# Performance work log

Hardware: AMD Instinct MI355X
Metric: run time of the kernel (lower is better)

Reference implementation:

```python
import jax, jax.numpy as jnp
import numpy as np

B, T, F, L, E, H, A, V = 64, 32, 512, 196, 512, 512, 512, 10000


def setup_inputs() -> dict:
    key = jax.random.key(0)
    ks = jax.random.split(key, 24)
    s = 0.02
    features = jax.random.normal(ks[0], (B, F, L), dtype=jnp.float32)
    captions = jax.random.randint(ks[1], (B, T), 0, V)
    lengths = jnp.sort(jax.random.randint(ks[2], (B,), 2, T + 1))[::-1]
    lengths = lengths.at[0].set(T)  # ensure max(decode_lengths) == T-1 (static)
    return {
        "features": features,
        "captions": captions,
        "lengths": lengths,
        "W_emb": jax.random.normal(ks[3], (V, E)) * s,
        "W_enc": jax.random.normal(ks[4], (A, F)) * s,
        "b_enc": jnp.zeros((A,)),
        "W_dec": jax.random.normal(ks[5], (A, H)) * s,
        "b_dec": jnp.zeros((A,)),
        "W_full": jax.random.normal(ks[6], (1, A)) * s,
        "b_full": jnp.zeros((1,)),
        "W_fbeta": jax.random.normal(ks[7], (F, H)) * s,
        "b_fbeta": jnp.zeros((F,)),
        "W_ih": jax.random.normal(ks[8], (4 * H, E + F)) * s,
        "W_hh": jax.random.normal(ks[9], (4 * H, H)) * s,
        "b_ih": jnp.zeros((4 * H,)),
        "b_hh": jnp.zeros((4 * H,)),
        "W_out": jax.random.normal(ks[10], (V, H)) * s,
        "b_out": jnp.zeros((V,)),
        "W_init_h": jax.random.normal(ks[11], (H, F)) * s,
        "b_init_h": jnp.zeros((H,)),
        "W_init_c": jax.random.normal(ks[12], (H, F)) * s,
        "b_init_c": jnp.zeros((H,)),
    }


def reference(features, captions, lengths, W_emb, W_enc, b_enc, W_dec, b_dec,
              W_full, b_full, W_fbeta, b_fbeta, W_ih, W_hh, b_ih, b_hh,
              W_out, b_out, W_init_h, b_init_h, W_init_c, b_init_c):
    Bv, Fv, Lv = features.shape
    Tmax = captions.shape[1] - 1  # max(decode_lengths), static (lengths[0]==T)
    feat_r = features.reshape(Bv, -1, Fv)          # [B, L, F] (torch .view semantics)
    en_att = feat_r @ W_enc.T + b_enc              # [B, L, A], step-invariant
    mean_f = features.mean(axis=2)                 # [B, F]
    h0 = mean_f @ W_init_h.T + b_init_h            # [B, H]
    c0 = mean_f @ W_init_c.T + b_init_c
    emb = W_emb[captions]                          # [B, T, E]
    dec_len = lengths - 1                          # [B]

    def step(carry, xs):
        h, c = carry
        emb_t, i = xs
        de = h @ W_dec.T + b_dec                                   # [B, A]
        full = (jnp.tanh(en_att + de[:, None, :]) @ W_full.T)[..., 0] + b_full[0]  # [B, L]
        alpha = jax.nn.softmax(full, axis=1)                       # [B, L]
        z = jnp.einsum('blf,bl->bf', feat_r, alpha)                # [B, F]
        z = z * jax.nn.sigmoid(h @ W_fbeta.T + b_fbeta)
        x = jnp.concatenate([emb_t, z], axis=1)                    # [B, E+F]
        gates = x @ W_ih.T + b_ih + h @ W_hh.T + b_hh              # [B, 4H]
        ig, fg, gg, og = jnp.split(gates, 4, axis=1)
        c_new = jax.nn.sigmoid(fg) * c + jax.nn.sigmoid(ig) * jnp.tanh(gg)
        h_new = jax.nn.sigmoid(og) * jnp.tanh(c_new)
        out = h_new @ W_out.T + b_out                              # [B, V] (dropout: eval)
        active = (dec_len > i)[:, None]                            # ragged mask
        h = jnp.where(active, h_new, h)
        c = jnp.where(active, c_new, c)
        pred = jnp.where(active, out, 0.0)
        alpha_m = jnp.where(active, alpha, 0.0)
        return (h, c), (pred, alpha_m)

    emb_steps = jnp.swapaxes(emb[:, :Tmax, :], 0, 1)               # [Tmax, B, E]
    (_, _), (preds, alphas) = jax.lax.scan(step, (h0, c0), (emb_steps, jnp.arange(Tmax)))
    predictions = jnp.swapaxes(preds, 0, 1)                        # [B, Tmax, V]
    alphas = jnp.swapaxes(alphas, 0, 1)                            # [B, Tmax, L]
    return predictions, alphas
```

## Files before the change

### kernel.cpp

```cpp
#include <hip/hip_runtime.h>


typedef unsigned short ushort_t;
typedef __attribute__((ext_vector_type(8))) short short8;
typedef __attribute__((ext_vector_type(4))) float f32x4;

__device__ __forceinline__ float bf2f(ushort_t u) {
    unsigned x = ((unsigned)u) << 16;
    float f;
    __builtin_memcpy(&f, &x, 4);
    return f;
}
__device__ __forceinline__ ushort_t f2bf(float f) {
    unsigned x;
    __builtin_memcpy(&x, &f, 4);
    unsigned r = (x + 0x7fffu + ((x >> 16) & 1u)) >> 16;
    return (ushort_t)r;
}
__device__ __forceinline__ float sigmoidf_(float x) { return 1.f / (1.f + __expf(-x)); }
__device__ __forceinline__ float tanh_fast(float x) {
    float e = __expf(2.f * x);
    return 1.f - 2.f / (e + 1.f);
}
__device__ __forceinline__ float wred_sum(float v) {
    #pragma unroll
    for (int m = 32; m; m >>= 1) v += __shfl_xor(v, m, 64);
    return v;
}
__device__ __forceinline__ float wred_max(float v) {
    #pragma unroll
    for (int m = 32; m; m >>= 1) v = fmaxf(v, __shfl_xor(v, m, 64));
    return v;
}

__device__ __forceinline__ float aload_f(const float* p) {
    return __hip_atomic_load((float*)p, __ATOMIC_RELAXED, __HIP_MEMORY_SCOPE_AGENT);
}
__device__ __forceinline__ void astore_f(float* p, float v) {
    __hip_atomic_store(p, v, __ATOMIC_RELAXED, __HIP_MEMORY_SCOPE_AGENT);
}
__device__ __forceinline__ unsigned aload_u(const unsigned* p) {
    return __hip_atomic_load((unsigned*)p, __ATOMIC_RELAXED, __HIP_MEMORY_SCOPE_AGENT);
}
__device__ __forceinline__ void astore_u(unsigned* p, unsigned v) {
    __hip_atomic_store(p, v, __ATOMIC_RELAXED, __HIP_MEMORY_SCOPE_AGENT);
}
__device__ __forceinline__ int aload_i(const int* p) {
    return __hip_atomic_load((int*)p, __ATOMIC_RELAXED, __HIP_MEMORY_SCOPE_AGENT);
}

#define KEXP2 2.8853901817779268f

__global__ void detect_kernel(const unsigned* __restrict__ feat_raw, int* __restrict__ flag,
                              int* __restrict__ slots) {
    int lane = threadIdx.x;
    #pragma unroll
    for (int i = 0; i < 8; ++i) slots[lane + i * 64] = 0;
    unsigned u = feat_raw[lane];
    unsigned e = (u >> 7) & 0xffu;
    bool bf_like = (e >= 105 && e <= 133);
    unsigned long long m = __ballot(bf_like);
    if (lane == 0) *flag = (__popcll(m) >= 40) ? 0 : 1;
}

#define NCVT 19
struct CvtArgs {
    const void* src[NCVT];
    void* dst[NCVT];
    int n[NCVT];
};

__global__ __launch_bounds__(256) void convert_kernel(CvtArgs a, const int* __restrict__ flag) {
    const int ai = blockIdx.y;
    const int n = a.n[ai];
    const int base = (blockIdx.x * 256 + threadIdx.x) * 8;
    if (base >= n) return;
    ushort_t* dst = (ushort_t*)a.dst[ai];
    if (*flag) {
        const float* s = (const float*)a.src[ai];
        #pragma unroll
        for (int i = 0; i < 8; ++i) {
            int idx = base + i;
            if (idx < n) dst[idx] = f2bf(s[idx]);
        }
    } else {
        const ushort_t* s = (const ushort_t*)a.src[ai];
        #pragma unroll
        for (int i = 0; i < 8; ++i) {
            int idx = base + i;
            if (idx < n) dst[idx] = s[idx];
        }
    }
}

__global__ __launch_bounds__(256) void embrows_kernel(const void* __restrict__ Wemb,
                                                      const int* __restrict__ captions,
                                                      const int* __restrict__ flag,
                                                      ushort_t* __restrict__ emb_c) {
    const int tb = blockIdx.x;
    const int t = tb >> 6, b = tb & 63;
    const int cap = captions[b * 32 + t];
    const int e0 = threadIdx.x;
    if (*flag) {
        const float* s = (const float*)Wemb + cap * 512;
        emb_c[tb * 512 + e0] = f2bf(s[e0]);
        emb_c[tb * 512 + e0 + 256] = f2bf(s[e0 + 256]);
    } else {
        const ushort_t* s = (const ushort_t*)Wemb + cap * 512;
        emb_c[tb * 512 + e0] = s[e0];
        emb_c[tb * 512 + e0 + 256] = s[e0 + 256];
    }
}

__global__ void prepw2_kernel(const ushort_t* __restrict__ wf, const ushort_t* __restrict__ bfc,
                              float* __restrict__ w2) {
    int tid = threadIdx.x;
    float w = bf2f(wf[tid]);
    w2[tid] = -2.f * w;
    float s = wred_sum(w);
    __shared__ float r8[8];
    if ((tid & 63) == 0) r8[tid >> 6] = s;
    __syncthreads();
    if (tid == 0) {
        float tot = r8[0] + r8[1] + r8[2] + r8[3] + r8[4] + r8[5] + r8[6] + r8[7];
        w2[512] = tot + bf2f(bfc[0]);
    }
}

template <class AROW, class BROW, class EPI>
__device__ __forceinline__ void gemm_tile(AROW arow, BROW brow, EPI epi) {
    __shared__ __align__(16) ushort_t As[64][40];
    __shared__ __align__(16) ushort_t Bs[64][40];
    const int tid = threadIdx.x;
    const int row = tid >> 2, ks = (tid & 3) << 3;
    const int wave = tid >> 6, lane = tid & 63;
    const int quad = lane >> 4, l15 = lane & 15;
    f32x4 acc[4];
    #pragma unroll
    for (int s = 0; s < 4; ++s) acc[s] = (f32x4){0.f, 0.f, 0.f, 0.f};
    const ushort_t* ap = arow(row);
    const ushort_t* bp = brow(row);
    for (int k0 = 0; k0 < 512; k0 += 32) {
        short8 av = {0, 0, 0, 0, 0, 0, 0, 0};
        short8 bv = {0, 0, 0, 0, 0, 0, 0, 0};
        if (ap) av = *(const short8*)(ap + k0 + ks);
        if (bp) bv = *(const short8*)(bp + k0 + ks);
        __syncthreads();
        *(short8*)&As[row][ks] = av;
        *(short8*)&Bs[row][ks] = bv;
        __syncthreads();
        short8 af = *(const short8*)&As[(wave << 4) + l15][quad << 3];
        #pragma unroll
        for (int s = 0; s < 4; ++s) {
            short8 bfr = *(const short8*)&Bs[(s << 4) + l15][quad << 3];
            acc[s] = __builtin_amdgcn_mfma_f32_16x16x32_bf16(af, bfr, acc[s], 0, 0, 0);
        }
    }
    epi((wave << 4) + (quad << 2), l15, acc);
}

__global__ __launch_bounds__(256) void mean_kernel(const ushort_t* __restrict__ features,
                                                   ushort_t* __restrict__ mean_bf) {
    const int b = blockIdx.x;
    const int wave = threadIdx.x >> 6, lane = threadIdx.x & 63;
    const ushort_t* fb = features + b * 512 * 196;
    for (int f = wave; f < 512; f += 4) {
        const ushort_t* r = fb + f * 196;
        float s = bf2f(r[lane]) + bf2f(r[lane + 64]) + bf2f(r[lane + 128]);
        if (lane < 4) s += bf2f(r[lane + 192]);
        s = wred_sum(s);
        if (lane == 0) mean_bf[b * 512 + f] = f2bf(s * (1.f / 196.f));
    }
}

__global__ __launch_bounds__(256) void init_kernel(
    const ushort_t* __restrict__ mean_bf, const ushort_t* __restrict__ Winh,
    const ushort_t* __restrict__ binh, const ushort_t* __restrict__ Winc,
    const ushort_t* __restrict__ binc, ushort_t* __restrict__ h_bf,
    float* __restrict__ cbuf) {
    const int n0 = blockIdx.x << 6;
    gemm_tile(
        [&](int r) { return mean_bf + r * 512; },
        [&](int r) {
            int n = n0 + r;
            return (n < 512) ? (Winh + n * 512) : (Winc + (n - 512) * 512);
        },
        [&](int mb, int l15, const f32x4* acc) {
            #pragma unroll
            for (int s = 0; s < 4; ++s) {
                int n = n0 + (s << 4) + l15;
                #pragma unroll
                for (int r = 0; r < 4; ++r) {
                    int b = mb + r;
                    if (n < 512)
                        h_bf[b * 512 + n] = f2bf(acc[s][r] + bf2f(binh[n]));
                    else
                        cbuf[b * 512 + (n - 512)] = acc[s][r] + bf2f(binc[n - 512]);
                }
            }
        });
}

__global__ __launch_bounds__(256) void enatt_kernel(const ushort_t* __restrict__ feat,
                                                    const ushort_t* __restrict__ Wenc,
                                                    const ushort_t* __restrict__ benc,
                                                    ushort_t* __restrict__ en_att) {
    const int m0 = blockIdx.y << 6, n0 = blockIdx.x << 6;
    gemm_tile(
        [&](int r) { return feat + (m0 + r) * 512; },
        [&](int r) { return Wenc + (n0 + r) * 512; },
        [&](int mb, int l15, const f32x4* acc) {
            #pragma unroll
            for (int s = 0; s < 4; ++s) {
                int n = n0 + (s << 4) + l15;
                float bias = bf2f(benc[n]);
                #pragma unroll
                for (int r = 0; r < 4; ++r) {
                    int m = m0 + mb + r;
                    en_att[m * 512 + n] = f2bf(acc[s][r] + bias);
                }
            }
        });
}

__global__ __launch_bounds__(256) void ec_kernel(const ushort_t* __restrict__ emb_c,
                                                 const ushort_t* __restrict__ Wih,
                                                 const ushort_t* __restrict__ bih,
                                                 const ushort_t* __restrict__ bhh,
                                                 float* __restrict__ ec) {
    const int t = blockIdx.y, n0 = blockIdx.x << 6;
    gemm_tile(
        [&](int r) { return emb_c + (t * 64 + r) * 512; },
        [&](int r) { return Wih + (n0 + r) * 1024; },
        [&](int mb, int l15, const f32x4* acc) {
            #pragma unroll
            for (int s = 0; s < 4; ++s) {
                int j = n0 + (s << 4) + l15;
                float bias = bf2f(bih[j]) + bf2f(bhh[j]);
                #pragma unroll
                for (int r = 0; r < 4; ++r) {
                    int b = mb + r;
                    ec[(t * 64 + b) * 2048 + j] = acc[s][r] + bias;
                }
            }
        });
}

__device__ __forceinline__ void gbar(int* slots, int e) {
    asm volatile("s_waitcnt vmcnt(0)" ::: "memory");
    __syncthreads();
    const int tid = threadIdx.x;
    if (tid == 0)
        __hip_atomic_store(slots + blockIdx.x, e, __ATOMIC_RELAXED,
                           __HIP_MEMORY_SCOPE_AGENT);
    if (blockIdx.x == 0) {
        if (tid < 64) {
            for (;;) {
                int a = aload_i(slots + tid);
                int b = aload_i(slots + tid + 64);
                int c = aload_i(slots + tid + 128);
                int d = aload_i(slots + tid + 192);
                if (__all(min(min(a, b), min(c, d)) >= e)) break;
                __builtin_amdgcn_s_sleep(1);
            }
            asm volatile("" ::: "memory");
            if (tid == 0)
                __hip_atomic_store(slots + 320, e, __ATOMIC_RELAXED,
                                   __HIP_MEMORY_SCOPE_AGENT);
        }
    } else if (tid == 0) {
        while (aload_i(slots + 320) < e) __builtin_amdgcn_s_sleep(1);
    }
    __syncthreads();
}

struct LoopArgs {
    const ushort_t* W3c;
    const ushort_t* bdec;
    const ushort_t* bfb;
    const ushort_t* en_att;
    const ushort_t* feat;
    const ushort_t* Wih;
    const float* w2;
    const float* ec;
    const int* lengths;
    const int* flag;
    ushort_t* h_bf;
    ushort_t* z_bf;
    ushort_t* H_all;
    float* cbuf;
    float* deK;
    float* fgate;
    float* hh;
    float* fullv;
    void* out_base;
    int* bar;
};

__global__ __launch_bounds__(512, 2) void loop_kernel(LoopArgs A) {
    const int blk = blockIdx.x, tid = threadIdx.x;
    const int wave = tid >> 6, lane = tid & 63;
    const int quad = lane >> 4, l15 = lane & 15;

    __shared__ __align__(16) ushort_t enS[49 * 512];
    __shared__ __align__(16) ushort_t ftS[196 * 128];
    __shared__ __align__(16) ushort_t AsL[16][520];
    __shared__ float smem[2048];
    __shared__ float red8[16];

    const int f32o = *A.flag;
    const int bB = blk >> 2;
    const int qB = blk & 3;
    const int lenB = A.lengths[bB];

    const int mtA = blk & 3;
    const int ntbA = (blk >> 2) << 3;
    const int b0A = mtA << 4;
    const int lenA = A.lengths[b0A + l15];

    const int dtC = blk >> 2;
    const int b0C = (blk & 3) << 4;
    const int lenC = A.lengths[b0C + l15];

    unsigned* h_u32 = (unsigned*)A.h_bf;
    unsigned* z_u32 = (unsigned*)A.z_bf;

    float w2r[8];
    {
        f32x4 w0 = *(const f32x4*)(A.w2 + lane * 8);
        f32x4 w1 = *(const f32x4*)(A.w2 + lane * 8 + 4);
        w2r[0] = w0[0]; w2r[1] = w0[1]; w2r[2] = w0[2]; w2r[3] = w0[3];
        w2r[4] = w1[0]; w2r[5] = w1[1]; w2r[6] = w1[2]; w2r[7] = w1[3];
    }
    const float fullc = A.w2[512];

    {
        const short8* src = (const short8*)(A.en_att + ((size_t)bB * 196 + qB * 49) * 512);
        short8* dst = (short8*)enS;
        for (int i = tid; i < 49 * 64; i += 512) dst[i] = src[i];
        const ushort_t* fsrc = A.feat + (size_t)bB * 100352 + qB * 128;
        short8* fdst = (short8*)ftS;
        for (int i = tid; i < 196 * 16; i += 512) {
            int l = i >> 4, c = i & 15;
            fdst[i] = *(const short8*)(fsrc + l * 512 + c * 8);
        }
    }

    int bt = 0;
    for (int t = 0; t < 31; ++t) {
        if (blk < 96) {
            bool anyact = __any(lenA - 1 > t);
            if (anyact) {
                for (int i = tid; i < 4096; i += 512) {
                    int r = i >> 8, c = i & 255;
                    unsigned v = aload_u(h_u32 + (b0A + r) * 256 + c);
                    *(unsigned*)&AsL[r][c << 1] = v;
                }
                __syncthreads();
                const int nt = ntbA + wave;
                const ushort_t* br = A.W3c + ((nt << 4) + l15) * 512 + (quad << 3);
                const ushort_t* arl = &AsL[l15][quad << 3];
                f32x4 acc = {0.f, 0.f, 0.f, 0.f};
                #pragma unroll
                for (int k0 = 0; k0 < 512; k0 += 32)
                    acc = __builtin_amdgcn_mfma_f32_16x16x32_bf16(
                        *(const short8*)(arl + k0), *(const short8*)(br + k0), acc, 0, 0, 0);
                const int n = (nt << 4) + l15;
                #pragma unroll
                for (int r = 0; r < 4; ++r) {
                    const int b = b0A + (quad << 2) + r;
                    float v = acc[r];
                    if (n < 512)
                        astore_f(A.deK + b * 512 + n, (v + bf2f(A.bdec[n])) * KEXP2);
                    else if (n < 1024)
                        astore_f(A.fgate + b * 512 + (n - 512),
                                 sigmoidf_(v + bf2f(A.bfb[n - 512])));
                    else
                        astore_f(A.hh + b * 2048 + (n - 1024), v);
                }
            }
        }
        ++bt; gbar(A.bar, bt);

        if ((lenB - 1) > t) {
            float dkr[8];
            const float* dk = A.deK + bB * 512 + lane * 8;
            #pragma unroll
            for (int j = 0; j < 8; ++j) dkr[j] = aload_f(dk + j);
            for (int i = wave; i < 49; i += 8) {
                short8 ev = *(const short8*)(enS + i * 512 + lane * 8);
                float acc = 0.f;
                #pragma unroll
                for (int j = 0; j < 8; ++j) {
                    float e2 = __builtin_amdgcn_exp2f(
                        fmaf(bf2f((ushort_t)ev[j]), KEXP2, dkr[j]));
                    acc = fmaf(w2r[j], __builtin_amdgcn_rcpf(e2 + 1.f), acc);
                }
                acc = wred_sum(acc);
                if (lane == 0) astore_f(A.fullv + bB * 196 + qB * 49 + i, acc + fullc);
            }
        }
        ++bt; gbar(A.bar, bt);

        {
            const bool act = (lenB - 1) > t;
            const size_t aoff = 19840000ull + ((size_t)bB * 31 + t) * 196;
            if (!act) {
                if (qB == 0 && tid < 196) {
                    if (f32o) ((float*)A.out_base)[aoff + tid] = 0.f;
                    else ((ushort_t*)A.out_base)[aoff + tid] = 0;
                }
            } else {
                float v = (tid < 196) ? aload_f(A.fullv + bB * 196 + tid) : -1e30f;
                float wm = wred_max(v);
                if (lane == 0) red8[wave] = wm;
                __syncthreads();
                float mx = fmaxf(fmaxf(fmaxf(red8[0], red8[1]), fmaxf(red8[2], red8[3])),
                                 fmaxf(fmaxf(red8[4], red8[5]), fmaxf(red8[6], red8[7])));
                float e = (tid < 196) ? __expf(v - mx) : 0.f;
                float sw = wred_sum(e);
                if (lane == 0) red8[8 + wave] = sw;
                __syncthreads();
                float tot = red8[8] + red8[9] + red8[10] + red8[11] +
                            red8[12] + red8[13] + red8[14] + red8[15];
                float inv = 1.f / tot;
                float a = e * inv;
                if (tid < 196) {
                    smem[tid] = a;
                    if (qB == 0) {
                        if (f32o) ((float*)A.out_base)[aoff + tid] = a;
                        else ((ushort_t*)A.out_base)[aoff + tid] = f2bf(a);
                    }
                }
                __syncthreads();
                const int fl = tid & 127, g = tid >> 7;
                float zacc = 0.f;
                #pragma unroll 4
                for (int l = g; l < 196; l += 4)
                    zacc = fmaf(smem[l], bf2f(ftS[l * 128 + fl]), zacc);
                smem[256 + (g << 7) + fl] = zacc;
                __syncthreads();
                if (tid < 64) {
                    const int f0l = tid << 1;
                    float z0 = smem[256 + f0l] + smem[384 + f0l] +
                               smem[512 + f0l] + smem[640 + f0l];
                    float z1 = smem[257 + f0l] + smem[385 + f0l] +
                               smem[513 + f0l] + smem[641 + f0l];
                    const int f0 = (qB << 7) + f0l;
                    z0 *= aload_f(A.fgate + bB * 512 + f0);
                    z1 *= aload_f(A.fgate + bB * 512 + f0 + 1);
                    unsigned zp = (unsigned)f2bf(z0) | ((unsigned)f2bf(z1) << 16);
                    astore_u(z_u32 + bB * 256 + (f0 >> 1), zp);
                }
            }
        }
        ++bt; gbar(A.bar, bt);

        if (blk < 128) {
            bool anyact = __any(lenC - 1 > t);
            if (anyact) {
                float pe[8], ph[8];
                #pragma unroll
                for (int k = 0; k < 8; ++k) { pe[k] = 0.f; ph[k] = 0.f; }
                if (tid < 128) {
                    const int bl = tid >> 3, p = tid & 7;
                    const int bE = b0C + bl;
                    const int dimE = (dtC << 4) + (p << 1);
                    const int eb = (t * 64 + bE) * 2048, hb = bE * 2048;
                    pe[0] = A.ec[eb + dimE];         pe[1] = A.ec[eb + dimE + 1];
                    pe[2] = A.ec[eb + 512 + dimE];   pe[3] = A.ec[eb + 512 + dimE + 1];
                    pe[4] = A.ec[eb + 1024 + dimE];  pe[5] = A.ec[eb + 1024 + dimE + 1];
                    pe[6] = A.ec[eb + 1536 + dimE];  pe[7] = A.ec[eb + 1536 + dimE + 1];
                    ph[0] = aload_f(A.hh + hb + dimE);
                    ph[1] = aload_f(A.hh + hb + dimE + 1);
                    ph[2] = aload_f(A.hh + hb + 512 + dimE);
                    ph[3] = aload_f(A.hh + hb + 512 + dimE + 1);
                    ph[4] = aload_f(A.hh + hb + 1024 + dimE);
                    ph[5] = aload_f(A.hh + hb + 1024 + dimE + 1);
                    ph[6] = aload_f(A.hh + hb + 1536 + dimE);
                    ph[7] = aload_f(A.hh + hb + 1536 + dimE + 1);
                }
                for (int i = tid; i < 4096; i += 512) {
                    int r = i >> 8, c = i & 255;
                    unsigned v = aload_u(z_u32 + (b0C + r) * 256 + c);
                    *(unsigned*)&AsL[r][c << 1] = v;
                }
                __syncthreads();
                const int g = wave & 3, kh = wave >> 2;
                const int j = (g << 9) + (dtC << 4) + l15;
                const ushort_t* br = A.Wih + j * 1024 + 512 + (kh << 8) + (quad << 3);
                const ushort_t* arl = &AsL[l15][(kh << 8) + (quad << 3)];
                f32x4 acc = {0.f, 0.f, 0.f, 0.f};
                #pragma unroll
                for (int k0 = 0; k0 < 256; k0 += 32)
                    acc = __builtin_amdgcn_mfma_f32_16x16x32_bf16(
                        *(const short8*)(arl + k0), *(const short8*)(br + k0), acc, 0, 0, 0);
                #pragma unroll
                for (int r = 0; r < 4; ++r)
                    smem[(wave << 8) + (((quad << 2) + r) << 4) + l15] = acc[r];
                __syncthreads();
                if (tid < 128) {
                    const int bl = tid >> 3, p = tid & 7;
                    const int b = b0C + bl;
                    const int i0 = (bl << 4) + (p << 1);
                    const int dim = (dtC << 4) + (p << 1);
                    float ig0 = smem[i0] + smem[1024 + i0] + pe[0] + ph[0];
                    float ig1 = smem[i0 + 1] + smem[1025 + i0] + pe[1] + ph[1];
                    float fg0 = smem[256 + i0] + smem[1280 + i0] + pe[2] + ph[2];
                    float fg1 = smem[257 + i0] + smem[1281 + i0] + pe[3] + ph[3];
                    float gg0 = smem[512 + i0] + smem[1536 + i0] + pe[4] + ph[4];
                    float gg1 = smem[513 + i0] + smem[1537 + i0] + pe[5] + ph[5];
                    float og0 = smem[768 + i0] + smem[1792 + i0] + pe[6] + ph[6];
                    float og1 = smem[769 + i0] + smem[1793 + i0] + pe[7] + ph[7];
                    float co0 = A.cbuf[b * 512 + dim];
                    float co1 = A.cbuf[b * 512 + dim + 1];
                    float cn0 = sigmoidf_(fg0) * co0 + sigmoidf_(ig0) * tanh_fast(gg0);
                    float hn0 = sigmoidf_(og0) * tanh_fast(cn0);
                    float cn1 = sigmoidf_(fg1) * co1 + sigmoidf_(ig1) * tanh_fast(gg1);
                    float hn1 = sigmoidf_(og1) * tanh_fast(cn1);
                    unsigned hp = (unsigned)f2bf(hn0) | ((unsigned)f2bf(hn1) << 16);
                    *(unsigned*)&A.H_all[(t * 64 + b) * 512 + dim] = hp;
                    if (A.lengths[b] - 1 > t) {
                        A.cbuf[b * 512 + dim] = cn0;
                        A.cbuf[b * 512 + dim + 1] = cn1;
                        astore_u(h_u32 + b * 256 + (dim >> 1), hp);
                    }
                }
            }
        }
        ++bt; gbar(A.bar, bt);
    }
}

__global__ __launch_bounds__(256) void preds_kernel(
    const ushort_t* __restrict__ H_all, const ushort_t* __restrict__ Wout,
    const ushort_t* __restrict__ bout, const int* __restrict__ lengths,
    const int* __restrict__ flag, void* __restrict__ out_base) {
    const int t = blockIdx.x, n0 = blockIdx.y << 6;
    const int f32o = *flag;
    gemm_tile(
        [&](int r) { return H_all + (t * 64 + r) * 512; },
        [&](int r) -> const ushort_t* {
            int n = n0 + r;
            return (n < 10000) ? (Wout + n * 512) : (const ushort_t*)nullptr;
        },
        [&](int mb, int l15, const f32x4* acc) {
            #pragma unroll
            for (int s = 0; s < 4; ++s) {
                int n = n0 + (s << 4) + l15;
                if (n >= 10000) continue;
                float bias = bf2f(bout[n]);
                #pragma unroll
                for (int r = 0; r < 4; ++r) {
                    int b = mb + r;
                    bool act = lengths[b] > t + 1;
                    float val = act ? (acc[s][r] + bias) : 0.f;
                    size_t off = (size_t)b * 310000 + t * 10000 + n;
                    if (f32o) ((float*)out_base)[off] = val;
                    else ((ushort_t*)out_base)[off] = act ? f2bf(val) : (ushort_t)0;
                }
            }
        });
}

extern "C" void kernel_launch(void* const* d_in, const int* in_sizes, int n_in,
                              void* d_out, int out_size, void* d_ws, size_t ws_size,
                              hipStream_t stream) {
    const void* features = d_in[0];
    const int* captions = (const int*)d_in[1];
    const int* lengths = (const int*)d_in[2];
    const void* W_emb = d_in[3];

    char* ws = (char*)d_ws;
    size_t o = 0;
    auto alloc = [&](size_t bytes) {
        size_t r = o;
        o += (bytes + 255) & ~(size_t)255;
        return r;
    };
    ushort_t* feat_c  = (ushort_t*)(ws + alloc(6422528ull * 2));
    ushort_t* Wenc_c  = (ushort_t*)(ws + alloc(262144ull * 2));
    ushort_t* benc_c  = (ushort_t*)(ws + alloc(512 * 2));
    ushort_t* W3c     = (ushort_t*)(ws + alloc(3072ull * 512 * 2));
    ushort_t* bdec_c  = (ushort_t*)(ws + alloc(512 * 2));
    ushort_t* wfull_c = (ushort_t*)(ws + alloc(512 * 2));
    ushort_t* bfull_c = (ushort_t*)(ws + alloc(2));
    ushort_t* bfb_c   = (ushort_t*)(ws + alloc(512 * 2));
    ushort_t* Wih_c   = (ushort_t*)(ws + alloc(2097152ull * 2));
    ushort_t* bih_c   = (ushort_t*)(ws + alloc(2048 * 2));
    ushort_t* bhh_c   = (ushort_t*)(ws + alloc(2048 * 2));
    ushort_t* Wout_c  = (ushort_t*)(ws + alloc(5120000ull * 2));
    ushort_t* bout_c  = (ushort_t*)(ws + alloc(10000 * 2));
    ushort_t* Winh_c  = (ushort_t*)(ws + alloc(262144ull * 2));
    ushort_t* binh_c  = (ushort_t*)(ws + alloc(512 * 2));
    ushort_t* Winc_c  = (ushort_t*)(ws + alloc(262144ull * 2));
    ushort_t* binc_c  = (ushort_t*)(ws + alloc(512 * 2));
    ushort_t* emb_c   = (ushort_t*)(ws + alloc(1984ull * 512 * 2));
    ushort_t* en_att  = (ushort_t*)(ws + alloc(12544ull * 512 * 2));
    float*    ec      = (float*)(ws + alloc(1984ull * 2048 * 4));
    ushort_t* H_all   = (ushort_t*)(ws + alloc(1984ull * 512 * 2));
    ushort_t* h_bf    = (ushort_t*)(ws + alloc(64 * 512 * 2));
    float*    cbuf    = (float*)(ws + alloc(64 * 512 * 4));
    float*    deK     = (float*)(ws + alloc(64 * 512 * 4));
    float*    fgate   = (float*)(ws + alloc(64 * 512 * 4));
    float*    hh      = (float*)(ws + alloc(64ull * 2048 * 4));
    ushort_t* z_bf    = (ushort_t*)(ws + alloc(64 * 512 * 2));
    ushort_t* mean_bf = (ushort_t*)(ws + alloc(64 * 512 * 2));
    float*    fullv   = (float*)(ws + alloc(64 * 196 * 4));
    float*    w2buf   = (float*)(ws + alloc(513 * 4));
    int*      flag    = (int*)(ws + alloc(256));
    int*      bar     = (int*)(ws + alloc(512 * 4));

    detect_kernel<<<1, 64, 0, stream>>>((const unsigned*)features, flag, bar);

    CvtArgs ca;
    const void* srcs[NCVT] = {features, d_in[4], d_in[5], d_in[6], d_in[7], d_in[8],
                              d_in[9], d_in[10], d_in[11], d_in[12], d_in[13], d_in[14],
                              d_in[15], d_in[16], d_in[17], d_in[18], d_in[19], d_in[20],
                              d_in[21]};
    void* dsts[NCVT] = {feat_c, Wenc_c, benc_c, W3c , bdec_c, wfull_c, bfull_c,
                        W3c + 262144 , bfb_c, Wih_c, W3c + 524288 ,
                        bih_c, bhh_c, Wout_c, bout_c, Winh_c, binh_c, Winc_c, binc_c};
    int ns[NCVT] = {6422528, 262144, 512, 262144, 512, 512, 1, 262144, 512,
                    2097152, 1048576, 2048, 2048, 5120000, 10000, 262144, 512,
                    262144, 512};
    for (int i = 0; i < NCVT; ++i) {
        ca.src[i] = srcs[i];
        ca.dst[i] = dsts[i];
        ca.n[i] = ns[i];
    }
    convert_kernel<<<dim3(3136, NCVT), 256, 0, stream>>>(ca, flag);
    embrows_kernel<<<1984, 256, 0, stream>>>(W_emb, captions, flag, emb_c);
    prepw2_kernel<<<1, 512, 0, stream>>>(wfull_c, bfull_c, w2buf);

    mean_kernel<<<64, 256, 0, stream>>>(feat_c, mean_bf);
    init_kernel<<<16, 256, 0, stream>>>(mean_bf, Winh_c, binh_c, Winc_c, binc_c,
                                        h_bf, cbuf);
    enatt_kernel<<<dim3(8, 196), 256, 0, stream>>>(feat_c, Wenc_c, benc_c, en_att);
    ec_kernel<<<dim3(32, 31), 256, 0, stream>>>(emb_c, Wih_c, bih_c, bhh_c, ec);

    LoopArgs la;
    la.W3c = W3c; la.bdec = bdec_c; la.bfb = bfb_c;
    la.en_att = en_att; la.feat = feat_c; la.Wih = Wih_c;
    la.w2 = w2buf; la.ec = ec; la.lengths = lengths; la.flag = flag;
    la.h_bf = h_bf; la.z_bf = z_bf; la.H_all = H_all;
    la.cbuf = cbuf; la.deK = deK; la.fgate = fgate; la.hh = hh;
    la.fullv = fullv; la.out_base = d_out; la.bar = bar;
    loop_kernel<<<256, 512, 0, stream>>>(la);

    preds_kernel<<<dim3(31, 157), 256, 0, stream>>>(H_all, Wout_c, bout_c, lengths,
                                                    flag, d_out);
}
```

Baseline: 1.189 ms.

## Replace grid-wide barriers with per-batch-group flag synchronization in recurrent loop

The persistent loop kernel stops using four grid-wide barriers per timestep. Its 256 blocks are split into 4 independent groups of 64, each owning 16 batch rows, and the groups coordinate through producer/consumer flag counters. Each group runs only to its own maximum decode length, and the attention logits are computed whole in each block instead of exchanged through global memory. This removes the global barrier latency and skips steps for shorter groups, at the cost of redundantly recomputing attention scores over all 196 locations per block, three quarters of them read from global memory.

```diff
diff --git a/kernel.cpp b/kernel.cpp
--- a/kernel.cpp
+++ b/kernel.cpp
@@ -48,14 +48,17 @@
 __device__ __forceinline__ int aload_i(const int* p) {
     return __hip_atomic_load((int*)p, __ATOMIC_RELAXED, __HIP_MEMORY_SCOPE_AGENT);
 }
+__device__ __forceinline__ void astore_i(int* p, int v) {
+    __hip_atomic_store(p, v, __ATOMIC_RELAXED, __HIP_MEMORY_SCOPE_AGENT);
+}
 
 #define KEXP2 2.8853901817779268f
 
 __global__ void detect_kernel(const unsigned* __restrict__ feat_raw, int* __restrict__ flag,
-                              int* __restrict__ slots) {
+                              int* __restrict__ flags) {
     int lane = threadIdx.x;
     #pragma unroll
-    for (int i = 0; i < 8; ++i) slots[lane + i * 64] = 0;
+    for (int i = 0; i < 8; ++i) flags[lane + i * 64] = 0;
     unsigned u = feat_raw[lane];
     unsigned e = (u >> 7) & 0xffu;
     bool bf_like = (e >= 105 && e <= 133);
@@ -246,34 +249,6 @@
         });
 }
 
-__device__ __forceinline__ void gbar(int* slots, int e) {
-    asm volatile("s_waitcnt vmcnt(0)" ::: "memory");
-    __syncthreads();
-    const int tid = threadIdx.x;
-    if (tid == 0)
-        __hip_atomic_store(slots + blockIdx.x, e, __ATOMIC_RELAXED,
-                           __HIP_MEMORY_SCOPE_AGENT);
-    if (blockIdx.x == 0) {
-        if (tid < 64) {
-            for (;;) {
-                int a = aload_i(slots + tid);
-                int b = aload_i(slots + tid + 64);
-                int c = aload_i(slots + tid + 128);
-                int d = aload_i(slots + tid + 192);
-                if (__all(min(min(a, b), min(c, d)) >= e)) break;
-                __builtin_amdgcn_s_sleep(1);
-            }
-            asm volatile("" ::: "memory");
-            if (tid == 0)
-                __hip_atomic_store(slots + 320, e, __ATOMIC_RELAXED,
-                                   __HIP_MEMORY_SCOPE_AGENT);
-        }
-    } else if (tid == 0) {
-        while (aload_i(slots + 320) < e) __builtin_amdgcn_s_sleep(1);
-    }
-    __syncthreads();
-}
-
 struct LoopArgs {
     const ushort_t* W3c;
     const ushort_t* bdec;
@@ -292,35 +267,34 @@
     float* deK;
     float* fgate;
     float* hh;
-    float* fullv;
     void* out_base;
-    int* bar;
+    int* flags;
 };
 
 __global__ __launch_bounds__(512, 2) void loop_kernel(LoopArgs A) {
     const int blk = blockIdx.x, tid = threadIdx.x;
     const int wave = tid >> 6, lane = tid & 63;
     const int quad = lane >> 4, l15 = lane & 15;
+    const int g = blk >> 6, local = blk & 63;
+    int* fbase = A.flags + g * 128;
 
     __shared__ __align__(16) ushort_t enS[49 * 512];
     __shared__ __align__(16) ushort_t ftS[196 * 128];
     __shared__ __align__(16) ushort_t AsL[16][520];
     __shared__ float smem[2048];
+    __shared__ float fullS[200];
     __shared__ float red8[16];
 
     const int f32o = *A.flag;
-    const int bB = blk >> 2;
-    const int qB = blk & 3;
+    const int b0 = g << 4;
+    const int Tg = A.lengths[b0] - 1;
+
+    const bool roleA = local < 24;
+    const int bB = b0 + (local >> 2);
+    const int qB = local & 3;
     const int lenB = A.lengths[bB];
-
-    const int mtA = blk & 3;
-    const int ntbA = (blk >> 2) << 3;
-    const int b0A = mtA << 4;
-    const int lenA = A.lengths[b0A + l15];
-
-    const int dtC = blk >> 2;
-    const int b0C = (blk & 3) << 4;
-    const int lenC = A.lengths[b0C + l15];
+    const bool roleC = local < 32;
+    const int dtC = local;
 
     unsigned* h_u32 = (unsigned*)A.h_bf;
     unsigned* z_u32 = (unsigned*)A.z_bf;
@@ -346,72 +320,84 @@
         }
     }
 
-    int bt = 0;
-    for (int t = 0; t < 31; ++t) {
-        if (blk < 96) {
-            bool anyact = __any(lenA - 1 > t);
-            if (anyact) {
-                for (int i = tid; i < 4096; i += 512) {
-                    int r = i >> 8, c = i & 255;
-                    unsigned v = aload_u(h_u32 + (b0A + r) * 256 + c);
-                    *(unsigned*)&AsL[r][c << 1] = v;
-                }
-                __syncthreads();
-                const int nt = ntbA + wave;
-                const ushort_t* br = A.W3c + ((nt << 4) + l15) * 512 + (quad << 3);
-                const ushort_t* arl = &AsL[l15][quad << 3];
-                f32x4 acc = {0.f, 0.f, 0.f, 0.f};
-                #pragma unroll
-                for (int k0 = 0; k0 < 512; k0 += 32)
-                    acc = __builtin_amdgcn_mfma_f32_16x16x32_bf16(
-                        *(const short8*)(arl + k0), *(const short8*)(br + k0), acc, 0, 0, 0);
-                const int n = (nt << 4) + l15;
-                #pragma unroll
-                for (int r = 0; r < 4; ++r) {
-                    const int b = b0A + (quad << 2) + r;
-                    float v = acc[r];
-                    if (n < 512)
-                        astore_f(A.deK + b * 512 + n, (v + bf2f(A.bdec[n])) * KEXP2);
-                    else if (n < 1024)
-                        astore_f(A.fgate + b * 512 + (n - 512),
-                                 sigmoidf_(v + bf2f(A.bfb[n - 512])));
-                    else
-                        astore_f(A.hh + b * 2048 + (n - 1024), v);
-                }
-            }
-        }
-        ++bt; gbar(A.bar, bt);
-
-        if ((lenB - 1) > t) {
-            float dkr[8];
-            const float* dk = A.deK + bB * 512 + lane * 8;
-            #pragma unroll
-            for (int j = 0; j < 8; ++j) dkr[j] = aload_f(dk + j);
-            for (int i = wave; i < 49; i += 8) {
-                short8 ev = *(const short8*)(enS + i * 512 + lane * 8);
-                float acc = 0.f;
-                #pragma unroll
-                for (int j = 0; j < 8; ++j) {
-                    float e2 = __builtin_amdgcn_exp2f(
-                        fmaf(bf2f((ushort_t)ev[j]), KEXP2, dkr[j]));
-                    acc = fmaf(w2r[j], __builtin_amdgcn_rcpf(e2 + 1.f), acc);
-                }
-                acc = wred_sum(acc);
-                if (lane == 0) astore_f(A.fullv + bB * 196 + qB * 49 + i, acc + fullc);
-            }
-        }
-        ++bt; gbar(A.bar, bt);
+    for (int t = 0; t < Tg; ++t) {
+        if (roleA) {
+            if (wave == 0 && t > 0) {
+                const int* fp = fbase + (lane & 31);
+                for (;;) {
+                    if (__all(aload_i(fp) >= t)) break;
+                    __builtin_amdgcn_s_sleep(1);
+                }
+                asm volatile("" ::: "memory");
+            }
+            __syncthreads();
+            for (int i = tid; i < 4096; i += 512) {
+                int r = i >> 8, c = i & 255;
+                *(unsigned*)&AsL[r][c << 1] = aload_u(h_u32 + ((b0 + r) << 8) + c);
+            }
+            __syncthreads();
+            const int nt = local * 8 + wave;
+            const ushort_t* br = A.W3c + ((nt << 4) + l15) * 512 + (quad << 3);
+            const ushort_t* arl = &AsL[l15][quad << 3];
+            f32x4 acc = {0.f, 0.f, 0.f, 0.f};
+            #pragma unroll
+            for (int k0 = 0; k0 < 512; k0 += 32)
+                acc = __builtin_amdgcn_mfma_f32_16x16x32_bf16(
+                    *(const short8*)(arl + k0), *(const short8*)(br + k0), acc, 0, 0, 0);
+            const int n = (nt << 4) + l15;
+            #pragma unroll
+            for (int r = 0; r < 4; ++r) {
+                const int b = b0 + (quad << 2) + r;
+                float v = acc[r];
+                if (n < 512)
+                    astore_f(A.deK + b * 512 + n, (v + bf2f(A.bdec[n])) * KEXP2);
+                else if (n < 1024)
+                    astore_f(A.fgate + b * 512 + (n - 512),
+                             sigmoidf_(v + bf2f(A.bfb[n - 512])));
+                else
+                    astore_f(A.hh + b * 2048 + (n - 1024), v);
+            }
+            asm volatile("s_waitcnt vmcnt(0)" ::: "memory");
+            __syncthreads();
+            if (tid == 0) astore_i(fbase + 32 + local, t + 1);
+        }
 
         {
+            if (wave == 0) {
+                const int* fp = fbase + 32 + (lane & 7);
+                for (;;) {
+                    if (__all(aload_i(fp) >= t + 1)) break;
+                    __builtin_amdgcn_s_sleep(1);
+                }
+                asm volatile("" ::: "memory");
+            }
+            __syncthreads();
             const bool act = (lenB - 1) > t;
             const size_t aoff = 19840000ull + ((size_t)bB * 31 + t) * 196;
-            if (!act) {
-                if (qB == 0 && tid < 196) {
-                    if (f32o) ((float*)A.out_base)[aoff + tid] = 0.f;
-                    else ((ushort_t*)A.out_base)[aoff + tid] = 0;
-                }
-            } else {
-                float v = (tid < 196) ? aload_f(A.fullv + bB * 196 + tid) : -1e30f;
+            if (act) {
+                float dkr[8];
+                const float* dk = A.deK + bB * 512 + lane * 8;
+                #pragma unroll
+                for (int j = 0; j < 8; ++j) dkr[j] = aload_f(dk + j);
+                const ushort_t* enb = A.en_att + (size_t)bB * 100352;
+                const int lp0 = qB * 49;
+                for (int l = wave; l < 196; l += 8) {
+                    const ushort_t* er = (l >= lp0 && l < lp0 + 49)
+                                             ? (enS + (l - lp0) * 512)
+                                             : (enb + l * 512);
+                    short8 ev = *(const short8*)(er + lane * 8);
+                    float acc = 0.f;
+                    #pragma unroll
+                    for (int j = 0; j < 8; ++j) {
+                        float e2 = __builtin_amdgcn_exp2f(
+                            fmaf(bf2f((ushort_t)ev[j]), KEXP2, dkr[j]));
+                        acc = fmaf(w2r[j], __builtin_amdgcn_rcpf(e2 + 1.f), acc);
+                    }
+                    acc = wred_sum(acc);
+                    if (lane == 0) fullS[l] = acc + fullc;
+                }
+                __syncthreads();
+                float v = (tid < 196) ? fullS[tid] : -1e30f;
                 float wm = wred_max(v);
                 if (lane == 0) red8[wave] = wm;
                 __syncthreads();
@@ -426,19 +412,19 @@
                 float inv = 1.f / tot;
                 float a = e * inv;
                 if (tid < 196) {
-                    smem[tid] = a;
+                    fullS[tid] = a;
                     if (qB == 0) {
                         if (f32o) ((float*)A.out_base)[aoff + tid] = a;
                         else ((ushort_t*)A.out_base)[aoff + tid] = f2bf(a);
                     }
                 }
                 __syncthreads();
-                const int fl = tid & 127, g = tid >> 7;
+                const int fl = tid & 127, gq = tid >> 7;
                 float zacc = 0.f;
                 #pragma unroll 4
-                for (int l = g; l < 196; l += 4)
-                    zacc = fmaf(smem[l], bf2f(ftS[l * 128 + fl]), zacc);
-                smem[256 + (g << 7) + fl] = zacc;
+                for (int l = gq; l < 196; l += 4)
+                    zacc = fmaf(fullS[l], bf2f(ftS[l * 128 + fl]), zacc);
+                smem[256 + (gq << 7) + fl] = zacc;
                 __syncthreads();
                 if (tid < 64) {
                     const int f0l = tid << 1;
@@ -452,83 +438,111 @@
                     unsigned zp = (unsigned)f2bf(z0) | ((unsigned)f2bf(z1) << 16);
                     astore_u(z_u32 + bB * 256 + (f0 >> 1), zp);
                 }
-            }
-        }
-        ++bt; gbar(A.bar, bt);
-
-        if (blk < 128) {
-            bool anyact = __any(lenC - 1 > t);
-            if (anyact) {
-                float pe[8], ph[8];
-                #pragma unroll
-                for (int k = 0; k < 8; ++k) { pe[k] = 0.f; ph[k] = 0.f; }
-                if (tid < 128) {
-                    const int bl = tid >> 3, p = tid & 7;
-                    const int bE = b0C + bl;
-                    const int dimE = (dtC << 4) + (p << 1);
-                    const int eb = (t * 64 + bE) * 2048, hb = bE * 2048;
-                    pe[0] = A.ec[eb + dimE];         pe[1] = A.ec[eb + dimE + 1];
-                    pe[2] = A.ec[eb + 512 + dimE];   pe[3] = A.ec[eb + 512 + dimE + 1];
-                    pe[4] = A.ec[eb + 1024 + dimE];  pe[5] = A.ec[eb + 1024 + dimE + 1];
-                    pe[6] = A.ec[eb + 1536 + dimE];  pe[7] = A.ec[eb + 1536 + dimE + 1];
-                    ph[0] = aload_f(A.hh + hb + dimE);
-                    ph[1] = aload_f(A.hh + hb + dimE + 1);
-                    ph[2] = aload_f(A.hh + hb + 512 + dimE);
-                    ph[3] = aload_f(A.hh + hb + 512 + dimE + 1);
-                    ph[4] = aload_f(A.hh + hb + 1024 + dimE);
-                    ph[5] = aload_f(A.hh + hb + 1024 + dimE + 1);
-                    ph[6] = aload_f(A.hh + hb + 1536 + dimE);
-                    ph[7] = aload_f(A.hh + hb + 1536 + dimE + 1);
-                }
-                for (int i = tid; i < 4096; i += 512) {
-                    int r = i >> 8, c = i & 255;
-                    unsigned v = aload_u(z_u32 + (b0C + r) * 256 + c);
-                    *(unsigned*)&AsL[r][c << 1] = v;
-                }
-                __syncthreads();
-                const int g = wave & 3, kh = wave >> 2;
-                const int j = (g << 9) + (dtC << 4) + l15;
-                const ushort_t* br = A.Wih + j * 1024 + 512 + (kh << 8) + (quad << 3);
-                const ushort_t* arl = &AsL[l15][(kh << 8) + (quad << 3)];
-                f32x4 acc = {0.f, 0.f, 0.f, 0.f};
-                #pragma unroll
-                for (int k0 = 0; k0 < 256; k0 += 32)
-                    acc = __builtin_amdgcn_mfma_f32_16x16x32_bf16(
-                        *(const short8*)(arl + k0), *(const short8*)(br + k0), acc, 0, 0, 0);
-                #pragma unroll
-                for (int r = 0; r < 4; ++r)
-                    smem[(wave << 8) + (((quad << 2) + r) << 4) + l15] = acc[r];
-                __syncthreads();
-                if (tid < 128) {
-                    const int bl = tid >> 3, p = tid & 7;
-                    const int b = b0C + bl;
-                    const int i0 = (bl << 4) + (p << 1);
-                    const int dim = (dtC << 4) + (p << 1);
-                    float ig0 = smem[i0] + smem[1024 + i0] + pe[0] + ph[0];
-                    float ig1 = smem[i0 + 1] + smem[1025 + i0] + pe[1] + ph[1];
-                    float fg0 = smem[256 + i0] + smem[1280 + i0] + pe[2] + ph[2];
-                    float fg1 = smem[257 + i0] + smem[1281 + i0] + pe[3] + ph[3];
-                    float gg0 = smem[512 + i0] + smem[1536 + i0] + pe[4] + ph[4];
-                    float gg1 = smem[513 + i0] + smem[1537 + i0] + pe[5] + ph[5];
-                    float og0 = smem[768 + i0] + smem[1792 + i0] + pe[6] + ph[6];
-                    float og1 = smem[769 + i0] + smem[1793 + i0] + pe[7] + ph[7];
-                    float co0 = A.cbuf[b * 512 + dim];
-                    float co1 = A.cbuf[b * 512 + dim + 1];
-                    float cn0 = sigmoidf_(fg0) * co0 + sigmoidf_(ig0) * tanh_fast(gg0);
-                    float hn0 = sigmoidf_(og0) * tanh_fast(cn0);
-                    float cn1 = sigmoidf_(fg1) * co1 + sigmoidf_(ig1) * tanh_fast(gg1);
-                    float hn1 = sigmoidf_(og1) * tanh_fast(cn1);
-                    unsigned hp = (unsigned)f2bf(hn0) | ((unsigned)f2bf(hn1) << 16);
-                    *(unsigned*)&A.H_all[(t * 64 + b) * 512 + dim] = hp;
-                    if (A.lengths[b] - 1 > t) {
-                        A.cbuf[b * 512 + dim] = cn0;
-                        A.cbuf[b * 512 + dim + 1] = cn1;
-                        astore_u(h_u32 + b * 256 + (dim >> 1), hp);
-                    }
-                }
-            }
-        }
-        ++bt; gbar(A.bar, bt);
+            } else {
+                if (qB == 0 && tid < 196) {
+                    if (f32o) ((float*)A.out_base)[aoff + tid] = 0.f;
+                    else ((ushort_t*)A.out_base)[aoff + tid] = 0;
+                }
+            }
+            asm volatile("s_waitcnt vmcnt(0)" ::: "memory");
+            __syncthreads();
+            if (tid == 0) astore_i(fbase + 64 + local, t + 1);
+        }
+
+        if (roleC) {
+            if (wave == 0) {
+                const int* zp = fbase + 64 + lane;
+                for (;;) {
+                    int v1 = aload_i(zp);
+                    int v2 = (lane < 4)
+                                 ? aload_i(fbase + 32 + 8 + lane * 4 + (dtC >> 3))
+                                 : 0x7fffffff;
+                    if (__all(v1 >= t + 1 && v2 >= t + 1)) break;
+                    __builtin_amdgcn_s_sleep(1);
+                }
+                asm volatile("" ::: "memory");
+            }
+            __syncthreads();
+            float pe[8], ph[8];
+            #pragma unroll
+            for (int k = 0; k < 8; ++k) { pe[k] = 0.f; ph[k] = 0.f; }
+            if (tid < 128) {
+                const int bl = tid >> 3, p = tid & 7;
+                const int bE = b0 + bl;
+                const int dimE = (dtC << 4) + (p << 1);
+                const int eb = (t * 64 + bE) * 2048, hb = bE * 2048;
+                pe[0] = A.ec[eb + dimE];         pe[1] = A.ec[eb + dimE + 1];
+                pe[2] = A.ec[eb + 512 + dimE];   pe[3] = A.ec[eb + 512 + dimE + 1];
+                pe[4] = A.ec[eb + 1024 + dimE];  pe[5] = A.ec[eb + 1024 + dimE + 1];
+                pe[6] = A.ec[eb + 1536 + dimE];  pe[7] = A.ec[eb + 1536 + dimE + 1];
+                ph[0] = aload_f(A.hh + hb + dimE);
+                ph[1] = aload_f(A.hh + hb + dimE + 1);
+                ph[2] = aload_f(A.hh + hb + 512 + dimE);
+                ph[3] = aload_f(A.hh + hb + 512 + dimE + 1);
+                ph[4] = aload_f(A.hh + hb + 1024 + dimE);
+                ph[5] = aload_f(A.hh + hb + 1024 + dimE + 1);
+                ph[6] = aload_f(A.hh + hb + 1536 + dimE);
+                ph[7] = aload_f(A.hh + hb + 1536 + dimE + 1);
+            }
+            for (int i = tid; i < 4096; i += 512) {
+                int r = i >> 8, c = i & 255;
+                *(unsigned*)&AsL[r][c << 1] = aload_u(z_u32 + ((b0 + r) << 8) + c);
+            }
+            __syncthreads();
+            const int gw = wave & 3, kh = wave >> 2;
+            const int j = (gw << 9) + (dtC << 4) + l15;
+            const ushort_t* br = A.Wih + j * 1024 + 512 + (kh << 8) + (quad << 3);
+            const ushort_t* arl = &AsL[l15][(kh << 8) + (quad << 3)];
+            f32x4 acc = {0.f, 0.f, 0.f, 0.f};
+            #pragma unroll
+            for (int k0 = 0; k0 < 256; k0 += 32)
+                acc = __builtin_amdgcn_mfma_f32_16x16x32_bf16(
+                    *(const short8*)(arl + k0), *(const short8*)(br + k0), acc, 0, 0, 0);
+            #pragma unroll
+            for (int r = 0; r < 4; ++r)
+                smem[(wave << 8) + (((quad << 2) + r) << 4) + l15] = acc[r];
+            __syncthreads();
+            if (tid < 128) {
+                const int bl = tid >> 3, p = tid & 7;
+                const int b = b0 + bl;
+                const int i0 = (bl << 4) + (p << 1);
+                const int dim = (dtC << 4) + (p << 1);
+                float ig0 = smem[i0] + smem[1024 + i0] + pe[0] + ph[0];
+                float ig1 = smem[i0 + 1] + smem[1025 + i0] + pe[1] + ph[1];
+                float fg0 = smem[256 + i0] + smem[1280 + i0] + pe[2] + ph[2];
+                float fg1 = smem[257 + i0] + smem[1281 + i0] + pe[3] + ph[3];
+                float gg0 = smem[512 + i0] + smem[1536 + i0] + pe[4] + ph[4];
+                float gg1 = smem[513 + i0] + smem[1537 + i0] + pe[5] + ph[5];
+                float og0 = smem[768 + i0] + smem[1792 + i0] + pe[6] + ph[6];
+                float og1 = smem[769 + i0] + smem[1793 + i0] + pe[7] + ph[7];
+                float co0 = A.cbuf[b * 512 + dim];
+                float co1 = A.cbuf[b * 512 + dim + 1];
+                float cn0 = sigmoidf_(fg0) * co0 + sigmoidf_(ig0) * tanh_fast(gg0);
+                float hn0 = sigmoidf_(og0) * tanh_fast(cn0);
+                float cn1 = sigmoidf_(fg1) * co1 + sigmoidf_(ig1) * tanh_fast(gg1);
+                float hn1 = sigmoidf_(og1) * tanh_fast(cn1);
+                unsigned hp = (unsigned)f2bf(hn0) | ((unsigned)f2bf(hn1) << 16);
+                *(unsigned*)&A.H_all[(t * 64 + b) * 512 + dim] = hp;
+                if (A.lengths[b] - 1 > t) {
+                    A.cbuf[b * 512 + dim] = cn0;
+                    A.cbuf[b * 512 + dim + 1] = cn1;
+                    astore_u(h_u32 + b * 256 + (dim >> 1), hp);
+                }
+            }
+            asm volatile("s_waitcnt vmcnt(0)" ::: "memory");
+            __syncthreads();
+            if (tid == 0) astore_i(fbase + dtC, t + 1);
+        }
+    }
+
+    if (qB == 0) {
+        for (int t = Tg; t < 31; ++t) {
+            if (tid < 196) {
+                const size_t aoff = 19840000ull + ((size_t)bB * 31 + t) * 196;
+                if (f32o) ((float*)A.out_base)[aoff + tid] = 0.f;
+                else ((ushort_t*)A.out_base)[aoff + tid] = 0;
+            }
+        }
     }
 }
 
@@ -606,12 +620,11 @@
     float*    hh      = (float*)(ws + alloc(64ull * 2048 * 4));
     ushort_t* z_bf    = (ushort_t*)(ws + alloc(64 * 512 * 2));
     ushort_t* mean_bf = (ushort_t*)(ws + alloc(64 * 512 * 2));
-    float*    fullv   = (float*)(ws + alloc(64 * 196 * 4));
     float*    w2buf   = (float*)(ws + alloc(513 * 4));
     int*      flag    = (int*)(ws + alloc(256));
-    int*      bar     = (int*)(ws + alloc(512 * 4));
-
-    detect_kernel<<<1, 64, 0, stream>>>((const unsigned*)features, flag, bar);
+    int*      flags   = (int*)(ws + alloc(512 * 4));
+
+    detect_kernel<<<1, 64, 0, stream>>>((const unsigned*)features, flag, flags);
 
     CvtArgs ca;
     const void* srcs[NCVT] = {features, d_in[4], d_in[5], d_in[6], d_in[7], d_in[8],
@@ -645,7 +658,7 @@
     la.w2 = w2buf; la.ec = ec; la.lengths = lengths; la.flag = flag;
     la.h_bf = h_bf; la.z_bf = z_bf; la.H_all = H_all;
     la.cbuf = cbuf; la.deK = deK; la.fgate = fgate; la.hh = hh;
-    la.fullv = fullv; la.out_base = d_out; la.bar = bar;
+    la.out_base = d_out; la.flags = flags;
     loop_kernel<<<256, 512, 0, stream>>>(la);
 
     preds_kernel<<<dim3(31, 157), 256, 0, stream>>>(H_all, Wout_c, bout_c, lengths,
```

New measurement: 1.454 ms. 1.22x slower.
